# Kernel tuning notes

Measured on AMD Instinct MI355X. Metric: run time of the kernel, lower is better.

The kernel has to match this reference:

```python
import jax, jax.numpy as jnp
import numpy as np

B, S, H, F, E, K = 2, 2048, 1024, 2816, 8, 2

def setup_inputs() -> dict:
    key = jax.random.key(0)
    k0, k1, k2, k3, k4 = jax.random.split(key, 5)
    return {
        "hidden_states": jax.random.normal(k0, (B, S, H), dtype=jnp.float32),
        "router_w": jax.random.normal(k1, (E, H), dtype=jnp.float32) * (1.0 / np.sqrt(H)),
        "w_gate": jax.random.normal(k2, (E, H, F), dtype=jnp.float32) * (1.0 / np.sqrt(H)),
        "w_up": jax.random.normal(k3, (E, H, F), dtype=jnp.float32) * (1.0 / np.sqrt(H)),
        "w_down": jax.random.normal(k4, (E, F, H), dtype=jnp.float32) * (1.0 / np.sqrt(F)),
    }

def reference(hidden_states, router_w, w_gate, w_up, w_down):
    # Router: logits [B,S,E], top-k routing with softmax over the k selected logits.
    router_logits = jnp.einsum("bsh,eh->bse", hidden_states, router_w)
    topk_values, topk_indices = jax.lax.top_k(router_logits, K)  # [B,S,K]
    topk_weights = jax.nn.softmax(topk_values.astype(jnp.float32), axis=-1).astype(hidden_states.dtype)

    x = hidden_states.reshape(-1, H)            # [T,H], T = B*S
    flat_idx = topk_indices.reshape(-1, K)      # [T,K] (int)
    flat_w = topk_weights.reshape(-1, K)        # [T,K]

    mixed = jnp.zeros_like(x)
    for e in range(E):  # small fixed expert loop; tokens fully vectorized
        # per-token combine weight for expert e (0 if not routed here)
        w_e = jnp.sum(jnp.where(flat_idx == e, flat_w, jnp.zeros_like(flat_w)), axis=-1)[:, None]
        # SwiGLU expert MLP: down(silu(gate(x)) * up(x))
        y = (jax.nn.silu(x @ w_gate[e]) * (x @ w_up[e])) @ w_down[e]
        mixed = mixed + w_e * y
    mixed_output = mixed.reshape(hidden_states.shape)

    # Load-balancing aux loss (Switch-style)
    router_probs = jax.nn.softmax(router_logits.astype(jnp.float32), axis=-1)
    P = router_probs.mean(axis=(0, 1))                                   # [E]
    f = jax.nn.one_hot(topk_indices, E, dtype=jnp.float32).mean(axis=(0, 1, 2))  # [E]
    aux_loss = E * jnp.sum(f * P)
    return mixed_output, aux_loss
```

## Files before the change

### kernel.cpp

```cpp
#include <hip/hip_runtime.h>
#include <hip/hip_bf16.h>
#include <stdint.h>

#define T_TOK 4096
#define H_DIM 1024
#define F_DIM 2816
#define E_NUM 8
#define ROWS_CAP 9216
#define TOTAL_MT 72

typedef float  f32x4  __attribute__((ext_vector_type(4)));
typedef __bf16 bf16x8 __attribute__((ext_vector_type(8)));

__device__ __forceinline__ unsigned short f32_bf16(float f) {
  union { float f; unsigned u; } v; v.f = f;
  unsigned r = v.u + 0x7fffu + ((v.u >> 16) & 1u);
  return (unsigned short)(r >> 16);
}

__device__ __forceinline__ void async16(const void* g, void* l) {
  __builtin_amdgcn_global_load_lds(
      (__attribute__((address_space(1))) void*)(g),
      (__attribute__((address_space(3))) void*)(l),
      16, 0, 0);
}

__device__ __forceinline__ f32x4 mfma16(bf16x8 a, bf16x8 b, f32x4 c) {
  return __builtin_amdgcn_mfma_f32_16x16x32_bf16(a, b, c, 0, 0, 0);
}


__global__ __launch_bounds__(256) void conv_x_kernel(const float* __restrict__ x,
                                                     unsigned short* __restrict__ xb) {
  int i = blockIdx.x * 256 + threadIdx.x;
  float4 v = ((const float4*)x)[i];
  ushort4 o;
  o.x = f32_bf16(v.x); o.y = f32_bf16(v.y); o.z = f32_bf16(v.z); o.w = f32_bf16(v.w);
  ((ushort4*)xb)[i] = o;
}

__global__ __launch_bounds__(256) void transpose_all(const float* __restrict__ wg,
                                                     const float* __restrict__ wu,
                                                     const float* __restrict__ wd,
                                                     unsigned short* __restrict__ Wgt,
                                                     unsigned short* __restrict__ Wut,
                                                     unsigned short* __restrict__ Wdt) {
  int bx = blockIdx.x;
  int mz = bx / 704, local = bx % 704;
  const float* s; unsigned short* d; int R, C, tx;
  size_t mat = (size_t)H_DIM * F_DIM;
  if (mz == 0)      { s = wg; d = Wgt; R = H_DIM; C = F_DIM; tx = 44; }
  else if (mz == 1) { s = wu; d = Wut; R = H_DIM; C = F_DIM; tx = 44; }
  else              { s = wd; d = Wdt; R = F_DIM; C = H_DIM; tx = 16; }
  int c0 = (local % tx) * 64;
  int rg0 = (local / tx) * 64;
  int e = blockIdx.y;
  s += e * mat; d += e * mat;
  int r0 = rg0;

  __shared__ float tile[64 * 65];
  int tid = threadIdx.x;
  int rr = tid >> 4, c4 = tid & 15;
#pragma unroll
  for (int it = 0; it < 4; it++) {
    int r = rr + 16 * it;
    float4 v = *(const float4*)(s + (size_t)(r0 + r) * C + c0 + c4 * 4);
    tile[r * 65 + c4 * 4 + 0] = v.x;
    tile[r * 65 + c4 * 4 + 1] = v.y;
    tile[r * 65 + c4 * 4 + 2] = v.z;
    tile[r * 65 + c4 * 4 + 3] = v.w;
  }
  __syncthreads();
  int cc = tid >> 4, r4 = tid & 15;
#pragma unroll
  for (int it = 0; it < 4; it++) {
    int c = cc + 16 * it;
    ushort4 o;
    o.x = f32_bf16(tile[(r4 * 4 + 0) * 65 + c]);
    o.y = f32_bf16(tile[(r4 * 4 + 1) * 65 + c]);
    o.z = f32_bf16(tile[(r4 * 4 + 2) * 65 + c]);
    o.w = f32_bf16(tile[(r4 * 4 + 3) * 65 + c]);
    *(ushort4*)(d + (size_t)(c0 + c) * R + r0 + r4 * 4) = o;
  }
}


__global__ __launch_bounds__(256) void router_kernel(const float* __restrict__ x,
                                                     const float* __restrict__ rw,
                                                     int* __restrict__ t2i,
                                                     float* __restrict__ t2w,
                                                     int* __restrict__ counts,
                                                     float* __restrict__ psum) {
  __shared__ float srw[E_NUM * H_DIM];
  __shared__ float sP[E_NUM];
  __shared__ int sC[E_NUM];
  int tid = threadIdx.x;
  for (int i = tid; i < E_NUM * H_DIM; i += 256) srw[i] = rw[i];
  if (tid < E_NUM) { sP[tid] = 0.f; sC[tid] = 0; }
  __syncthreads();
  int w = tid >> 6, lane = tid & 63;
  for (int it = 0; it < 4; ++it) {
    int t = blockIdx.x * 16 + w * 4 + it;
    float acc[E_NUM];
#pragma unroll
    for (int e = 0; e < E_NUM; e++) acc[e] = 0.f;
    const float* xr = x + (size_t)t * H_DIM;
    for (int h = lane; h < H_DIM; h += 64) {
      float xv = xr[h];
#pragma unroll
      for (int e = 0; e < E_NUM; e++) acc[e] += xv * srw[e * H_DIM + h];
    }
#pragma unroll
    for (int e = 0; e < E_NUM; e++) {
      float v = acc[e];
      for (int o = 32; o > 0; o >>= 1) v += __shfl_down(v, o, 64);
      acc[e] = __shfl(v, 0, 64);
    }
    if (lane == 0) {
      float mx = acc[0];
#pragma unroll
      for (int e = 1; e < E_NUM; e++) mx = fmaxf(mx, acc[e]);
      float pr[E_NUM], s = 0.f;
#pragma unroll
      for (int e = 0; e < E_NUM; e++) { pr[e] = __expf(acc[e] - mx); s += pr[e]; }
      float inv = 1.f / s;
#pragma unroll
      for (int e = 0; e < E_NUM; e++) atomicAdd(&sP[e], pr[e] * inv);
      int i0 = 0; float v0 = acc[0];
#pragma unroll
      for (int e = 1; e < E_NUM; e++) if (acc[e] > v0) { v0 = acc[e]; i0 = e; }
      int i1 = -1; float v1 = -3.4e38f;
#pragma unroll
      for (int e = 0; e < E_NUM; e++) if (e != i0 && acc[e] > v1) { v1 = acc[e]; i1 = e; }
      float e1 = __expf(v1 - v0);
      float w0 = 1.f / (1.f + e1);
      t2i[2 * t] = i0; t2i[2 * t + 1] = i1;
      t2w[2 * t] = w0; t2w[2 * t + 1] = e1 * w0;
      atomicAdd(&sC[i0], 1); atomicAdd(&sC[i1], 1);
    }
  }
  __syncthreads();
  if (tid < E_NUM) { atomicAdd(&counts[tid], sC[tid]); atomicAdd(&psum[tid], sP[tid]); }
}

__global__ void scan_aux_kernel(const int* __restrict__ counts, const float* __restrict__ psum,
                                int* __restrict__ offsets, int* __restrict__ cursors,
                                float* __restrict__ aux_out) {
  if (threadIdx.x == 0 && blockIdx.x == 0) {
    int off = 0; float aux = 0.f;
    for (int e = 0; e < E_NUM; e++) {
      offsets[e] = off;
      cursors[e] = off;
      off += (counts[e] + 127) & ~127;
      aux += ((float)counts[e] / 8192.0f) * (psum[e] / 4096.0f);
    }
    offsets[E_NUM] = off;
    *aux_out = 8.0f * aux;
  }
}

__global__ __launch_bounds__(256) void assign_kernel(const int* __restrict__ t2i,
                                                     const float* __restrict__ t2w,
                                                     int* __restrict__ cursors,
                                                     int* __restrict__ row2token,
                                                     float* __restrict__ roww,
                                                     int* __restrict__ t2row) {
  int t = blockIdx.x * 256 + threadIdx.x;
#pragma unroll
  for (int s = 0; s < 2; s++) {
    int e = t2i[2 * t + s];
    int p = atomicAdd(&cursors[e], 1);
    row2token[p] = t;
    roww[p] = t2w[2 * t + s];
    t2row[2 * t + s] = p;
  }
}

__device__ __forceinline__ int find_expert(const int* __restrict__ offsets, int row0,
                                           int& off_out) {
  int esel = -1, off = 0;
#pragma unroll
  for (int e = 0; e < E_NUM; e++) {
    int lo = offsets[e], hi = offsets[e + 1];
    if (row0 >= lo && row0 < hi) { esel = e; off = lo; }
  }
  off_out = off;
  return esel;
}

__global__ __launch_bounds__(256) void gateup_kernel(
    const unsigned short* __restrict__ xb,
    const unsigned short* __restrict__ wgt,
    const unsigned short* __restrict__ wut,
    unsigned short* __restrict__ act,
    const int* __restrict__ counts, const int* __restrict__ offsets,
    const int* __restrict__ row2token) {
  int g = blockIdx.x;
  int row0 = g * 128;
  int off;
  int e = find_expert(offsets, row0, off);
  if (e < 0) return;
  int cnt = counts[e];
  int rowbase = row0 - off;
  int ntile = blockIdx.y;

  __shared__ __align__(16) unsigned short smA[128 * 32];
  __shared__ __align__(16) unsigned short smG[64 * 32];
  __shared__ __align__(16) unsigned short smU[64 * 32];

  int tid = threadIdx.x;
  int w = tid >> 6, lane = tid & 63;
  int wm = w & 1, wn = w >> 1;

  int cA0 = w * 64 + lane;
  int rA0 = cA0 >> 2, qA0 = cA0 & 3;
  int rA1 = rA0 + 64;
  int tok0 = (rowbase + rA0 < cnt) ? row2token[off + rowbase + rA0] : 0;
  int tok1 = (rowbase + rA1 < cnt) ? row2token[off + rowbase + rA1] : 0;
  const unsigned short* gA0 = xb + (size_t)tok0 * H_DIM + qA0 * 8;
  const unsigned short* gA1 = xb + (size_t)tok1 * H_DIM + qA0 * 8;
  size_t wb = (size_t)e * F_DIM * H_DIM;
  const unsigned short* gG = wgt + wb + (size_t)(ntile * 64 + rA0) * H_DIM + qA0 * 8;
  const unsigned short* gU = wut + wb + (size_t)(ntile * 64 + rA0) * H_DIM + qA0 * 8;
  unsigned short* lA0 = smA + (w * 64) * 8;
  unsigned short* lA1 = smA + (256 + w * 64) * 8;
  unsigned short* lG = smG + (w * 64) * 8;
  unsigned short* lU = smU + (w * 64) * 8;

  f32x4 accg[4][2], accu[4][2];
#pragma unroll
  for (int i = 0; i < 4; i++)
#pragma unroll
    for (int j = 0; j < 2; j++) {
      accg[i][j] = (f32x4){0.f, 0.f, 0.f, 0.f};
      accu[i][j] = (f32x4){0.f, 0.f, 0.f, 0.f};
    }

  int m = lane & 15, quad = lane >> 4;
  for (int k0 = 0; k0 < H_DIM; k0 += 32) {
    async16(gA0 + k0, lA0);
    async16(gA1 + k0, lA1);
    async16(gG + k0, lG);
    async16(gU + k0, lU);
    __syncthreads();
    bf16x8 a[4], bg[2], bu[2];
#pragma unroll
    for (int i = 0; i < 4; i++)
      a[i] = *(const bf16x8*)(smA + (wm * 64 + 16 * i + m) * 32 + quad * 8);
#pragma unroll
    for (int j = 0; j < 2; j++) {
      bg[j] = *(const bf16x8*)(smG + (wn * 32 + 16 * j + m) * 32 + quad * 8);
      bu[j] = *(const bf16x8*)(smU + (wn * 32 + 16 * j + m) * 32 + quad * 8);
    }
#pragma unroll
    for (int i = 0; i < 4; i++)
#pragma unroll
      for (int j = 0; j < 2; j++) {
        accg[i][j] = mfma16(a[i], bg[j], accg[i][j]);
        accu[i][j] = mfma16(a[i], bu[j], accu[i][j]);
      }
    __syncthreads();
  }

#pragma unroll
  for (int i = 0; i < 4; i++)
#pragma unroll
    for (int j = 0; j < 2; j++)
#pragma unroll
      for (int r = 0; r < 4; r++) {
        int rt = wm * 64 + 16 * i + quad * 4 + r;
        int ct = wn * 32 + 16 * j + m;
        float g2 = accg[i][j][r], u = accu[i][j][r];
        float sv = g2 / (1.f + __expf(-g2)) * u;
        act[(size_t)(off + rowbase + rt) * F_DIM + ntile * 64 + ct] = f32_bf16(sv);
      }
}

__global__ __launch_bounds__(256) void down_kernel(
    const unsigned short* __restrict__ act,
    const unsigned short* __restrict__ wdt,
    const int* __restrict__ counts, const int* __restrict__ offsets,
    const float* __restrict__ roww,
    float* __restrict__ Y) {
  int g = blockIdx.x;
  int row0 = g * 128;
  int off;
  int e = find_expert(offsets, row0, off);
  if (e < 0) return;
  int cnt = counts[e];
  int rowbase = row0 - off;
  int ntile = blockIdx.y;
  int ks = blockIdx.z;
  int kbase = ks * (F_DIM / 2);

  __shared__ __align__(16) unsigned short smA[128 * 32];
  __shared__ __align__(16) unsigned short smB[128 * 32];

  int tid = threadIdx.x;
  int w = tid >> 6, lane = tid & 63;
  int wm = w & 1, wn = w >> 1;

  int r0 = tid >> 2, q0 = tid & 3;
  int r1 = r0 + 64;
  const unsigned short* gA0 = act + (size_t)(off + rowbase + r0) * F_DIM + kbase + q0 * 8;
  const unsigned short* gA1 = act + (size_t)(off + rowbase + r1) * F_DIM + kbase + q0 * 8;
  size_t wb = (size_t)e * H_DIM * F_DIM;
  const unsigned short* gB0 = wdt + wb + (size_t)(ntile * 128 + r0) * F_DIM + kbase + q0 * 8;
  const unsigned short* gB1 = wdt + wb + (size_t)(ntile * 128 + r1) * F_DIM + kbase + q0 * 8;
  unsigned short* lA0 = smA + tid * 8;
  unsigned short* lA1 = smA + (tid + 256) * 8;
  unsigned short* lB0 = smB + tid * 8;
  unsigned short* lB1 = smB + (tid + 256) * 8;

  f32x4 acc[4][4];
#pragma unroll
  for (int i = 0; i < 4; i++)
#pragma unroll
    for (int j = 0; j < 4; j++) acc[i][j] = (f32x4){0.f, 0.f, 0.f, 0.f};

  int m = lane & 15, quad = lane >> 4;
  for (int k0 = 0; k0 < F_DIM / 2; k0 += 32) {
    async16(gA0 + k0, lA0);
    async16(gA1 + k0, lA1);
    async16(gB0 + k0, lB0);
    async16(gB1 + k0, lB1);
    __syncthreads();
    bf16x8 a[4], b[4];
#pragma unroll
    for (int i = 0; i < 4; i++) {
      a[i] = *(const bf16x8*)(smA + (wm * 64 + 16 * i + m) * 32 + quad * 8);
      b[i] = *(const bf16x8*)(smB + (wn * 64 + 16 * i + m) * 32 + quad * 8);
    }
#pragma unroll
    for (int i = 0; i < 4; i++)
#pragma unroll
      for (int j = 0; j < 4; j++) acc[i][j] = mfma16(a[i], b[j], acc[i][j]);
    __syncthreads();
  }

  float* Yk = Y + (size_t)ks * ROWS_CAP * H_DIM;
#pragma unroll
  for (int i = 0; i < 4; i++)
#pragma unroll
    for (int r = 0; r < 4; r++) {
      int rt = wm * 64 + 16 * i + quad * 4 + r;
      int lrow = rowbase + rt;
      if (lrow < cnt) {
        float cw = roww[off + lrow];
#pragma unroll
        for (int j = 0; j < 4; j++) {
          int h = ntile * 128 + wn * 64 + 16 * j + m;
          Yk[(size_t)(off + lrow) * H_DIM + h] = cw * acc[i][j][r];
        }
      }
    }
}

__global__ __launch_bounds__(256) void combine_kernel(const float* __restrict__ Y,
                                                      const int* __restrict__ t2row,
                                                      float* __restrict__ out) {
  int t = blockIdx.x, hc = threadIdx.x;
  int r0 = t2row[2 * t], r1 = t2row[2 * t + 1];
  const float* Y1 = Y + (size_t)ROWS_CAP * H_DIM;
  float4 a = ((const float4*)(Y  + (size_t)r0 * H_DIM))[hc];
  float4 b = ((const float4*)(Y  + (size_t)r1 * H_DIM))[hc];
  float4 c = ((const float4*)(Y1 + (size_t)r0 * H_DIM))[hc];
  float4 d = ((const float4*)(Y1 + (size_t)r1 * H_DIM))[hc];
  float4 o;
  o.x = (a.x + b.x) + (c.x + d.x);
  o.y = (a.y + b.y) + (c.y + d.y);
  o.z = (a.z + b.z) + (c.z + d.z);
  o.w = (a.w + b.w) + (c.w + d.w);
  ((float4*)(out + (size_t)t * H_DIM))[hc] = o;
}


extern "C" void kernel_launch(void* const* d_in, const int* in_sizes, int n_in,
                              void* d_out, int out_size, void* d_ws, size_t ws_size,
                              hipStream_t stream) {
  const float* x  = (const float*)d_in[0];
  const float* rw = (const float*)d_in[1];
  const float* wg = (const float*)d_in[2];
  const float* wu = (const float*)d_in[3];
  const float* wd = (const float*)d_in[4];
  float* out = (float*)d_out;

  char* ws = (char*)d_ws;
  size_t p = 0;
  auto alloc = [&](size_t bytes) {
    char* r = ws + p;
    p = (p + bytes + 255) & ~(size_t)255;
    return r;
  };
  unsigned short* Xb  = (unsigned short*)alloc((size_t)T_TOK * H_DIM * 2);
  unsigned short* Wgt = (unsigned short*)alloc((size_t)E_NUM * F_DIM * H_DIM * 2);
  unsigned short* Wut = (unsigned short*)alloc((size_t)E_NUM * F_DIM * H_DIM * 2);
  unsigned short* Wdt = (unsigned short*)alloc((size_t)E_NUM * H_DIM * F_DIM * 2);
  unsigned short* Act = (unsigned short*)alloc((size_t)ROWS_CAP * F_DIM * 2);
  int*   t2i = (int*)alloc(T_TOK * 2 * 4);
  float* t2w = (float*)alloc(T_TOK * 2 * 4);
  int*   t2row = (int*)alloc(T_TOK * 2 * 4);
  int*   row2token = (int*)alloc(ROWS_CAP * 4);
  float* roww = (float*)alloc(ROWS_CAP * 4);
  int* ctrs = (int*)alloc(64 * 4);
  int* counts  = ctrs;
  int* cursors = ctrs + 8;
  float* psum  = (float*)(ctrs + 16);
  int* offsets = ctrs + 24;
  float* Y = (float*)Wgt;

  hipMemsetAsync(ctrs, 0, 96, stream);

  conv_x_kernel<<<T_TOK * H_DIM / 4 / 256, 256, 0, stream>>>(x, Xb);
  transpose_all<<<dim3(2112, E_NUM), 256, 0, stream>>>(wg, wu, wd, Wgt, Wut, Wdt);

  router_kernel<<<T_TOK / 16, 256, 0, stream>>>(x, rw, t2i, t2w, counts, psum);
  scan_aux_kernel<<<1, 64, 0, stream>>>(counts, psum, offsets, cursors, out + (size_t)T_TOK * H_DIM);
  assign_kernel<<<T_TOK / 256, 256, 0, stream>>>(t2i, t2w, cursors, row2token, roww, t2row);

  gateup_kernel<<<dim3(TOTAL_MT, F_DIM / 64), 256, 0, stream>>>(Xb, Wgt, Wut, Act, counts, offsets, row2token);
  down_kernel<<<dim3(TOTAL_MT, H_DIM / 128, 2), 256, 0, stream>>>(Act, Wdt, counts, offsets, roww, Y);
  combine_kernel<<<T_TOK, 256, 0, stream>>>(Y, t2row, out);
}
```

Measured before the change: 626.2 us.

## XOR-swizzle LDS tiles, widen gate/up K-step to 64, vectorize transpose stores

Applies an XOR swizzle to the shared-memory layout of the A and B tiles in both GEMM kernels, so that the 16-byte fragment reads by MFMA lanes land in different LDS banks. The gate/up kernel also doubles its K tile to 64, which halves the number of barrier pairs per output tile at the cost of more LDS. The weight transpose now writes 16-byte vectors instead of 8-byte ones. The risks are the higher LDS footprint limiting occupancy and the swizzle index math adding integer ops.

```diff
diff --git a/kernel.cpp b/kernel.cpp
--- a/kernel.cpp
+++ b/kernel.cpp
@@ -11,6 +11,7 @@
 
 typedef float  f32x4  __attribute__((ext_vector_type(4)));
 typedef __bf16 bf16x8 __attribute__((ext_vector_type(8)));
+typedef unsigned short ushort8_t __attribute__((ext_vector_type(8)));
 
 __device__ __forceinline__ unsigned short f32_bf16(float f) {
   union { float f; unsigned u; } v; v.f = f;
@@ -52,11 +53,10 @@
   if (mz == 0)      { s = wg; d = Wgt; R = H_DIM; C = F_DIM; tx = 44; }
   else if (mz == 1) { s = wu; d = Wut; R = H_DIM; C = F_DIM; tx = 44; }
   else              { s = wd; d = Wdt; R = F_DIM; C = H_DIM; tx = 16; }
-  int c0 = (local % tx) * 64;
-  int rg0 = (local / tx) * 64;
   int e = blockIdx.y;
   s += e * mat; d += e * mat;
-  int r0 = rg0;
+  int c0 = (local % tx) * 64;
+  int r0 = (local / tx) * 64;
 
   __shared__ float tile[64 * 65];
   int tid = threadIdx.x;
@@ -71,16 +71,14 @@
     tile[r * 65 + c4 * 4 + 3] = v.w;
   }
   __syncthreads();
-  int cc = tid >> 4, r4 = tid & 15;
-#pragma unroll
-  for (int it = 0; it < 4; it++) {
-    int c = cc + 16 * it;
-    ushort4 o;
-    o.x = f32_bf16(tile[(r4 * 4 + 0) * 65 + c]);
-    o.y = f32_bf16(tile[(r4 * 4 + 1) * 65 + c]);
-    o.z = f32_bf16(tile[(r4 * 4 + 2) * 65 + c]);
-    o.w = f32_bf16(tile[(r4 * 4 + 3) * 65 + c]);
-    *(ushort4*)(d + (size_t)(c0 + c) * R + r0 + r4 * 4) = o;
+#pragma unroll
+  for (int it = 0; it < 2; it++) {
+    int c = tid + it * 256;
+    int col = c >> 3, q = c & 7;
+    ushort8_t o;
+#pragma unroll
+    for (int k = 0; k < 8; k++) o[k] = f32_bf16(tile[(q * 8 + k) * 65 + col]);
+    *(ushort8_t*)(d + (size_t)(c0 + col) * R + r0 + q * 8) = o;
   }
 }
 
@@ -204,28 +202,37 @@
   int rowbase = row0 - off;
   int ntile = blockIdx.y;
 
-  __shared__ __align__(16) unsigned short smA[128 * 32];
-  __shared__ __align__(16) unsigned short smG[64 * 32];
-  __shared__ __align__(16) unsigned short smU[64 * 32];
+  __shared__ __align__(16) unsigned short smA[128 * 64];
+  __shared__ __align__(16) unsigned short smG[64 * 64];
+  __shared__ __align__(16) unsigned short smU[64 * 64];
 
   int tid = threadIdx.x;
   int w = tid >> 6, lane = tid & 63;
   int wm = w & 1, wn = w >> 1;
 
-  int cA0 = w * 64 + lane;
-  int rA0 = cA0 >> 2, qA0 = cA0 & 3;
-  int rA1 = rA0 + 64;
-  int tok0 = (rowbase + rA0 < cnt) ? row2token[off + rowbase + rA0] : 0;
-  int tok1 = (rowbase + rA1 < cnt) ? row2token[off + rowbase + rA1] : 0;
-  const unsigned short* gA0 = xb + (size_t)tok0 * H_DIM + qA0 * 8;
-  const unsigned short* gA1 = xb + (size_t)tok1 * H_DIM + qA0 * 8;
+  const unsigned short* gA[4]; unsigned short* lA[4];
   size_t wb = (size_t)e * F_DIM * H_DIM;
-  const unsigned short* gG = wgt + wb + (size_t)(ntile * 64 + rA0) * H_DIM + qA0 * 8;
-  const unsigned short* gU = wut + wb + (size_t)(ntile * 64 + rA0) * H_DIM + qA0 * 8;
-  unsigned short* lA0 = smA + (w * 64) * 8;
-  unsigned short* lA1 = smA + (256 + w * 64) * 8;
-  unsigned short* lG = smG + (w * 64) * 8;
-  unsigned short* lU = smU + (w * 64) * 8;
+#pragma unroll
+  for (int i = 0; i < 4; i++) {
+    int c = tid + i * 256;
+    int r = c >> 3, qs = c & 7;
+    int q = qs ^ (r & 7);
+    int tok = (rowbase + r < cnt) ? row2token[off + rowbase + r] : 0;
+    gA[i] = xb + (size_t)tok * H_DIM + q * 8;
+    lA[i] = smA + c * 8;
+  }
+  const unsigned short* gG[2]; const unsigned short* gU[2];
+  unsigned short* lG[2]; unsigned short* lU[2];
+#pragma unroll
+  for (int i = 0; i < 2; i++) {
+    int c = tid + i * 256;
+    int r = c >> 3, qs = c & 7;
+    int q = qs ^ (r & 7);
+    gG[i] = wgt + wb + (size_t)(ntile * 64 + r) * H_DIM + q * 8;
+    gU[i] = wut + wb + (size_t)(ntile * 64 + r) * H_DIM + q * 8;
+    lG[i] = smG + c * 8;
+    lU[i] = smU + c * 8;
+  }
 
   f32x4 accg[4][2], accu[4][2];
 #pragma unroll
@@ -237,28 +244,38 @@
     }
 
   int m = lane & 15, quad = lane >> 4;
-  for (int k0 = 0; k0 < H_DIM; k0 += 32) {
-    async16(gA0 + k0, lA0);
-    async16(gA1 + k0, lA1);
-    async16(gG + k0, lG);
-    async16(gU + k0, lU);
+  for (int k0 = 0; k0 < H_DIM; k0 += 64) {
+#pragma unroll
+    for (int i = 0; i < 4; i++) async16(gA[i] + k0, lA[i]);
+#pragma unroll
+    for (int i = 0; i < 2; i++) {
+      async16(gG[i] + k0, lG[i]);
+      async16(gU[i] + k0, lU[i]);
+    }
     __syncthreads();
-    bf16x8 a[4], bg[2], bu[2];
-#pragma unroll
-    for (int i = 0; i < 4; i++)
-      a[i] = *(const bf16x8*)(smA + (wm * 64 + 16 * i + m) * 32 + quad * 8);
-#pragma unroll
-    for (int j = 0; j < 2; j++) {
-      bg[j] = *(const bf16x8*)(smG + (wn * 32 + 16 * j + m) * 32 + quad * 8);
-      bu[j] = *(const bf16x8*)(smU + (wn * 32 + 16 * j + m) * 32 + quad * 8);
-    }
-#pragma unroll
-    for (int i = 0; i < 4; i++)
+#pragma unroll
+    for (int h = 0; h < 2; h++) {
+      bf16x8 a[4], bg[2], bu[2];
+#pragma unroll
+      for (int i = 0; i < 4; i++) {
+        int row = wm * 64 + 16 * i + m;
+        a[i] = *(const bf16x8*)(smA + row * 64 + (((h * 4 + quad) ^ (row & 7)) * 8));
+      }
 #pragma unroll
       for (int j = 0; j < 2; j++) {
-        accg[i][j] = mfma16(a[i], bg[j], accg[i][j]);
-        accu[i][j] = mfma16(a[i], bu[j], accu[i][j]);
+        int row = wn * 32 + 16 * j + m;
+        int o = row * 64 + (((h * 4 + quad) ^ (row & 7)) * 8);
+        bg[j] = *(const bf16x8*)(smG + o);
+        bu[j] = *(const bf16x8*)(smU + o);
       }
+#pragma unroll
+      for (int i = 0; i < 4; i++)
+#pragma unroll
+        for (int j = 0; j < 2; j++) {
+          accg[i][j] = mfma16(a[i], bg[j], accg[i][j]);
+          accu[i][j] = mfma16(a[i], bu[j], accu[i][j]);
+        }
+    }
     __syncthreads();
   }
 
@@ -300,17 +317,19 @@
   int w = tid >> 6, lane = tid & 63;
   int wm = w & 1, wn = w >> 1;
 
-  int r0 = tid >> 2, q0 = tid & 3;
-  int r1 = r0 + 64;
-  const unsigned short* gA0 = act + (size_t)(off + rowbase + r0) * F_DIM + kbase + q0 * 8;
-  const unsigned short* gA1 = act + (size_t)(off + rowbase + r1) * F_DIM + kbase + q0 * 8;
+  const unsigned short* gA[2]; const unsigned short* gB[2];
+  unsigned short* lA[2]; unsigned short* lB[2];
   size_t wb = (size_t)e * H_DIM * F_DIM;
-  const unsigned short* gB0 = wdt + wb + (size_t)(ntile * 128 + r0) * F_DIM + kbase + q0 * 8;
-  const unsigned short* gB1 = wdt + wb + (size_t)(ntile * 128 + r1) * F_DIM + kbase + q0 * 8;
-  unsigned short* lA0 = smA + tid * 8;
-  unsigned short* lA1 = smA + (tid + 256) * 8;
-  unsigned short* lB0 = smB + tid * 8;
-  unsigned short* lB1 = smB + (tid + 256) * 8;
+#pragma unroll
+  for (int i = 0; i < 2; i++) {
+    int c = tid + i * 256;
+    int r = c >> 2, qs = c & 3;
+    int q = qs ^ (r & 3);
+    gA[i] = act + (size_t)(off + rowbase + r) * F_DIM + kbase + q * 8;
+    gB[i] = wdt + wb + (size_t)(ntile * 128 + r) * F_DIM + kbase + q * 8;
+    lA[i] = smA + c * 8;
+    lB[i] = smB + c * 8;
+  }
 
   f32x4 acc[4][4];
 #pragma unroll
@@ -320,16 +339,19 @@
 
   int m = lane & 15, quad = lane >> 4;
   for (int k0 = 0; k0 < F_DIM / 2; k0 += 32) {
-    async16(gA0 + k0, lA0);
-    async16(gA1 + k0, lA1);
-    async16(gB0 + k0, lB0);
-    async16(gB1 + k0, lB1);
+#pragma unroll
+    for (int i = 0; i < 2; i++) {
+      async16(gA[i] + k0, lA[i]);
+      async16(gB[i] + k0, lB[i]);
+    }
     __syncthreads();
     bf16x8 a[4], b[4];
 #pragma unroll
     for (int i = 0; i < 4; i++) {
-      a[i] = *(const bf16x8*)(smA + (wm * 64 + 16 * i + m) * 32 + quad * 8);
-      b[i] = *(const bf16x8*)(smB + (wn * 64 + 16 * i + m) * 32 + quad * 8);
+      int rowa = wm * 64 + 16 * i + m;
+      int rowb = wn * 64 + 16 * i + m;
+      a[i] = *(const bf16x8*)(smA + rowa * 32 + ((quad ^ (rowa & 3)) * 8));
+      b[i] = *(const bf16x8*)(smB + rowb * 32 + ((quad ^ (rowb & 3)) * 8));
     }
 #pragma unroll
     for (int i = 0; i < 4; i++)
```

Result: no change. 627.2 us (+0.2%).
